# Performance work log

Measured on AMD Instinct MI355X. Metric: run time of the kernel, lower is better.

Reference implementation:

```python
import jax, jax.numpy as jnp
import numpy as np

B, T, D, H = 2, 2048, 1024, 16  # batch, seq_len, d_model (d_in==d_out), num_heads
HD = D // H  # head_dim = 64


def setup_inputs() -> dict:
    key = jax.random.key(0)
    ks = jax.random.split(key, 6)
    s = 1.0 / np.sqrt(D)
    return {
        "x": jax.random.normal(ks[0], (B, T, D), dtype=jnp.float32),
        "wq": jax.random.normal(ks[1], (D, D), dtype=jnp.float32) * s,
        "wk": jax.random.normal(ks[2], (D, D), dtype=jnp.float32) * s,
        "wv": jax.random.normal(ks[3], (D, D), dtype=jnp.float32) * s,
        "wo": jax.random.normal(ks[4], (D, D), dtype=jnp.float32) * s,
        "bo": jax.random.normal(ks[5], (D,), dtype=jnp.float32) * 0.01,
    }


def reference(x, wq, wk, wv, wo, bo):
    b, t, d = x.shape
    # projections (qkv_bias=False), split heads: [b, h, t, hd]
    q = (x @ wq).reshape(b, t, H, HD).transpose(0, 2, 1, 3)
    k = (x @ wk).reshape(b, t, H, HD).transpose(0, 2, 1, 3)
    v = (x @ wv).reshape(b, t, H, HD).transpose(0, 2, 1, 3)
    # causal attention scores [b, h, t, t]
    scores = jnp.einsum("bhqd,bhkd->bhqk", q, k) / jnp.sqrt(jnp.float32(HD))
    causal = jnp.tril(jnp.ones((t, t), dtype=bool))
    scores = jnp.where(causal[None, None, :, :], scores, -jnp.inf)
    attn = jax.nn.softmax(scores, axis=-1)  # dropout p=0.0 -> identity
    ctx = jnp.einsum("bhqk,bhkd->bhqd", attn, v)  # [b, h, t, hd]
    ctx = ctx.transpose(0, 2, 1, 3).reshape(b, t, d)  # merge heads
    return ctx @ wo + bo
```

## Files before the change

### kernel.cpp

```cpp
#include <hip/hip_runtime.h>
#include <hip/hip_bf16.h>
#include <stdint.h>

#define B_  2
#define T_  2048
#define D_  1024
#define H_  16
#define HD_ 64

typedef __bf16 bf16x8 __attribute__((ext_vector_type(8)));
typedef __bf16 bf16x4 __attribute__((ext_vector_type(4)));
typedef float  f32x4  __attribute__((ext_vector_type(4)));

__device__ __forceinline__ void async_copy16(const void* g, void* l) {
  __builtin_amdgcn_global_load_lds((__attribute__((address_space(1))) void*)(g),
                                   (__attribute__((address_space(3))) void*)(l),
                                   16, 0, 0);
}

__global__ void prep_kernel(const float* __restrict__ x,
                            const float* __restrict__ wq, const float* __restrict__ wk,
                            const float* __restrict__ wv, const float* __restrict__ wo,
                            __bf16* __restrict__ xc,
                            __bf16* __restrict__ wqkv_t, __bf16* __restrict__ wo_t) {
  const int id  = blockIdx.x;
  const int tid = threadIdx.x;
  if (id < 4096) {
    __shared__ __bf16 tile[32][33];
    const int z   = id >> 10;
    const int rem = id & 1023;
    const int n0 = (rem & 31) * 32, k0 = (rem >> 5) * 32;
    const int tx = tid & 31, ty = tid >> 5;
    const float* src = (z == 0) ? wq : (z == 1) ? wk : (z == 2) ? wv : wo;
    __bf16* dst = (z < 3) ? (wqkv_t + (size_t)z * 1024 * 1024) : wo_t;
#pragma unroll
    for (int i = 0; i < 4; ++i)
      tile[ty + 8 * i][tx] = (__bf16)src[(size_t)(k0 + ty + 8 * i) * 1024 + n0 + tx];
    __syncthreads();
#pragma unroll
    for (int i = 0; i < 4; ++i)
      dst[(size_t)(n0 + ty + 8 * i) * 1024 + k0 + tx] = tile[tx][ty + 8 * i];
  } else {
    const int i0 = ((id - 4096) * 256 + tid) * 4;
    const f32x4 f = *(const f32x4*)(x + i0);
    bf16x4 v;
#pragma unroll
    for (int k = 0; k < 4; ++k) v[k] = (__bf16)f[k];
    *(bf16x4*)(xc + i0) = v;
  }
}

template <int MODE>
__launch_bounds__(256)
__global__ void gemm128_kernel(const __bf16* __restrict__ A, const __bf16* __restrict__ Bt, int K,
                               __bf16* __restrict__ q_b, __bf16* __restrict__ k_b,
                               __bf16* __restrict__ vt_b,
                               const float* __restrict__ bo, float* __restrict__ outp) {
  __shared__ __align__(16) __bf16 As[128 * 64];
  __shared__ __align__(16) __bf16 Bs[128 * 64];
  const int tid  = threadIdx.x;
  const int w    = tid >> 6, lane = tid & 63;
  const int quad = lane >> 4, lr = lane & 15;

  const int orig = blockIdx.x;
  int bx, by;
  if (MODE == 0) {
    const int wgid = (orig & 7) * 96 + (orig >> 3);
    bx = wgid >> 5;
    by = wgid & 31;
  } else {
    const int wgid = (orig & 7) * 32 + (orig >> 3);
    bx = wgid & 7;
    by = wgid >> 3;
  }
  const int tm = by * 128, tn = bx * 128;
  const int wm = (w >> 1) * 64, wn = (w & 1) * 64;
  const int lrow   = lane >> 3;
  const int gchunk = (lane & 7) ^ lrow;

  f32x4 acc[4][4] = {};

  for (int k0 = 0; k0 < K; k0 += 64) {
#pragma unroll
    for (int c = 0; c < 4; ++c) {
      const int chunk = w * 4 + c;
      const int row   = chunk * 8 + lrow;
      async_copy16(A  + (size_t)(tm + row) * K + k0 + gchunk * 8, As + chunk * 512);
      async_copy16(Bt + (size_t)(tn + row) * K + k0 + gchunk * 8, Bs + chunk * 512);
    }
    __syncthreads();
#pragma unroll
    for (int ks = 0; ks < 2; ++ks) {
      bf16x8 af[4], bfr[4];
#pragma unroll
      for (int mi = 0; mi < 4; ++mi) {
        const int row = wm + mi * 16 + lr;
        const int ch  = (ks * 4 + quad) ^ (row & 7);
        af[mi] = *(const bf16x8*)(As + row * 64 + ch * 8);
      }
#pragma unroll
      for (int ni = 0; ni < 4; ++ni) {
        const int row = wn + ni * 16 + lr;
        const int ch  = (ks * 4 + quad) ^ (row & 7);
        bfr[ni] = *(const bf16x8*)(Bs + row * 64 + ch * 8);
      }
#pragma unroll
      for (int mi = 0; mi < 4; ++mi)
#pragma unroll
        for (int ni = 0; ni < 4; ++ni)
          acc[mi][ni] = __builtin_amdgcn_mfma_f32_16x16x32_bf16(af[mi], bfr[ni], acc[mi][ni], 0, 0, 0);
    }
    __syncthreads();
  }

  if (MODE == 0) {
#pragma unroll
    for (int mi = 0; mi < 4; ++mi) {
      const int mrow0 = tm + wm + mi * 16 + quad * 4;
      const int b  = mrow0 >> 11;
      const int t0 = mrow0 & 2047;
#pragma unroll
      for (int ni = 0; ni < 4; ++ni) {
        const int ncol = tn + wn + ni * 16 + lr;
        const int mat  = ncol >> 10;
        const int nn   = ncol & 1023;
        const int h = nn >> 6, hd = nn & 63;
        if (mat == 0) {
#pragma unroll
          for (int r = 0; r < 4; ++r)
            q_b[((size_t)((b * H_ + h) * T_ + t0 + r)) * HD_ + hd] =
                (__bf16)(acc[mi][ni][r] * 0.125f);
        } else if (mat == 1) {
#pragma unroll
          for (int r = 0; r < 4; ++r)
            k_b[((size_t)((b * H_ + h) * T_ + t0 + r)) * HD_ + hd] =
                (__bf16)(acc[mi][ni][r]);
        } else {
          bf16x4 pk;
#pragma unroll
          for (int r = 0; r < 4; ++r) pk[r] = (__bf16)(acc[mi][ni][r]);
          *(bf16x4*)(vt_b + ((size_t)(b * H_ + h) * HD_ + hd) * T_ + t0) = pk;
        }
      }
    }
  } else {
#pragma unroll
    for (int mi = 0; mi < 4; ++mi) {
      const int m0 = tm + wm + mi * 16 + quad * 4;
#pragma unroll
      for (int ni = 0; ni < 4; ++ni) {
        const int n = tn + wn + ni * 16 + lr;
        const float bias = bo[n];
#pragma unroll
        for (int r = 0; r < 4; ++r)
          outp[(size_t)(m0 + r) * D_ + n] = acc[mi][ni][r] + bias;
      }
    }
  }
}

__launch_bounds__(256, 3)
__global__ void attn_kernel(const __bf16* __restrict__ q_b, const __bf16* __restrict__ k_b,
                            const __bf16* __restrict__ vt_b, __bf16* __restrict__ ctx) {
  __shared__ __align__(16) __bf16 sV[64 * 64];
  __shared__ __align__(16) __bf16 sP[2][64][72];
  const int tid  = threadIdx.x;
  const int w    = tid >> 6, lane = tid & 63;
  const int quad = lane >> 4, lr = lane & 15;
  const int id = blockIdx.x;
  const int bh  = (id & 7) * 4 + ((id >> 3) & 3);
  const int t0i = (id >> 5) & 7;
  const int rnd = id >> 8;
  const int tq  = (3 - rnd) * 8 + ((rnd & 1) ? t0i : (7 - t0i));
  const __bf16* qh = q_b  + (size_t)bh * T_ * HD_;
  const __bf16* kh = k_b  + (size_t)bh * T_ * HD_;
  const __bf16* vh = vt_b + (size_t)bh * HD_ * T_;
  const int b = bh >> 4, h = bh & 15;

  const int r0 = tid >> 3, r1 = (tid + 256) >> 3;
  const int g0 = tid & 7;

  const int q0 = tq * 64;
  const int nj = tq + 1;
  const int w16 = w * 16;

  bf16x8 qf[4][2];
#pragma unroll
  for (int qs = 0; qs < 4; ++qs)
#pragma unroll
    for (int ks = 0; ks < 2; ++ks)
      qf[qs][ks] = *(const bf16x8*)(qh + (size_t)(q0 + qs * 16 + lr) * HD_ + ks * 32 + quad * 8);

  bf16x8 onesf;
#pragma unroll
  for (int j = 0; j < 8; ++j) onesf[j] = (__bf16)1.0f;

  f32x4 o[4] = {};
  f32x4 ls = {};

  const __bf16* kr = kh + (size_t)(w16 + lr) * HD_;
  bf16x8 kf0 = *(const bf16x8*)(kr + quad * 8);
  bf16x8 kf1 = *(const bf16x8*)(kr + 32 + quad * 8);
  bf16x8 kn0, kn1;

  bf16x8 vr0 = *(const bf16x8*)(vh + (size_t)r0 * T_ + g0 * 8);
  bf16x8 vr1 = *(const bf16x8*)(vh + (size_t)r1 * T_ + g0 * 8);

  for (int j = 0; j < nj; ++j) {
    const int j0 = j * 64;
    const int pb = j & 1;
    __syncthreads();
    *(bf16x8*)(sV + r0 * 64 + (g0 ^ (r0 & 7)) * 8) = vr0;
    *(bf16x8*)(sV + r1 * 64 + (g0 ^ (r1 & 7)) * 8) = vr1;
    __syncthreads();
    if (j + 1 < nj) {
      const int jn = j0 + 64;
      vr0 = *(const bf16x8*)(vh + (size_t)r0 * T_ + jn + g0 * 8);
      vr1 = *(const bf16x8*)(vh + (size_t)r1 * T_ + jn + g0 * 8);
      kn0 = *(const bf16x8*)(kr + (size_t)jn * HD_ + quad * 8);
      kn1 = *(const bf16x8*)(kr + (size_t)jn * HD_ + 32 + quad * 8);
    }
    f32x4 ns[4] = {};
    __builtin_amdgcn_s_setprio(1);
#pragma unroll
    for (int qb = 0; qb < 4; ++qb) {
      ns[qb] = __builtin_amdgcn_mfma_f32_16x16x32_bf16(kf0, qf[qb][0], ns[qb], 0, 0, 0);
      ns[qb] = __builtin_amdgcn_mfma_f32_16x16x32_bf16(kf1, qf[qb][1], ns[qb], 0, 0, 0);
    }
    __builtin_amdgcn_s_setprio(0);
    if (j + 1 < nj) { kf0 = kn0; kf1 = kn1; }
    if (j0 + 63 > q0) {
      const int kvb = j0 + w16 + quad * 4;
#pragma unroll
      for (int qb = 0; qb < 4; ++qb) {
        const int qg = q0 + qb * 16 + lr;
#pragma unroll
        for (int r = 0; r < 4; ++r)
          if (kvb + r > qg) ns[qb][r] = -3.0e38f;
      }
    }
#pragma unroll
    for (int qb = 0; qb < 4; ++qb)
#pragma unroll
      for (int r = 0; r < 4; ++r)
        ns[qb][r] = __expf(ns[qb][r]);
#pragma unroll
    for (int qb = 0; qb < 4; ++qb) {
      bf16x4 pk;
#pragma unroll
      for (int r = 0; r < 4; ++r) pk[r] = (__bf16)ns[qb][r];
      *(bf16x4*)(&sP[pb][qb * 16 + lr][w16 + quad * 4]) = pk;
    }
    __syncthreads();
    bf16x8 pf[2];
#pragma unroll
    for (int ks = 0; ks < 2; ++ks)
      pf[ks] = *(const bf16x8*)(&sP[pb][w16 + lr][ks * 32 + quad * 8]);
    __builtin_amdgcn_s_setprio(1);
#pragma unroll
    for (int ni = 0; ni < 4; ++ni) {
      const int row = ni * 16 + lr;
#pragma unroll
      for (int ks = 0; ks < 2; ++ks) {
        const int ch = (ks * 4 + quad) ^ (row & 7);
        bf16x8 vf = *(const bf16x8*)(sV + row * 64 + ch * 8);
        o[ni] = __builtin_amdgcn_mfma_f32_16x16x32_bf16(pf[ks], vf, o[ni], 0, 0, 0);
      }
    }
    ls = __builtin_amdgcn_mfma_f32_16x16x32_bf16(pf[0], onesf, ls, 0, 0, 0);
    ls = __builtin_amdgcn_mfma_f32_16x16x32_bf16(pf[1], onesf, ls, 0, 0, 0);
    __builtin_amdgcn_s_setprio(0);
  }
#pragma unroll
  for (int r = 0; r < 4; ++r) {
    const float inv = 1.0f / ls[r];
    const int t = q0 + w16 + quad * 4 + r;
#pragma unroll
    for (int ni = 0; ni < 4; ++ni)
      ctx[((size_t)(b * T_ + t)) * D_ + h * HD_ + ni * 16 + lr] =
          (__bf16)(o[ni][r] * inv);
  }
}

extern "C" void kernel_launch(void* const* d_in, const int* in_sizes, int n_in,
                              void* d_out, int out_size, void* d_ws, size_t ws_size,
                              hipStream_t stream) {
  (void)in_sizes; (void)n_in; (void)out_size; (void)ws_size;
  const float* x  = (const float*)d_in[0];
  const float* wq = (const float*)d_in[1];
  const float* wk = (const float*)d_in[2];
  const float* wv = (const float*)d_in[3];
  const float* wo = (const float*)d_in[4];
  const float* bo = (const float*)d_in[5];
  float* outp = (float*)d_out;

  char* ws = (char*)d_ws;
  __bf16* ctx    = (__bf16*)(ws + 0);
  __bf16* wqkv_t = (__bf16*)(ws + 0);
  __bf16* wo_t   = (__bf16*)(ws + 8388608);
  __bf16* q_b    = (__bf16*)(ws + 10485760);
  __bf16* k_b    = (__bf16*)(ws + 18874368);
  __bf16* vt_b   = (__bf16*)(ws + 27262976);
  __bf16* xc     = (__bf16*)(ws + 35651584);

  prep_kernel<<<8192, 256, 0, stream>>>(x, wq, wk, wv, wo, xc, wqkv_t, wo_t);
  gemm128_kernel<0><<<768, 256, 0, stream>>>(xc, wqkv_t, 1024, q_b, k_b, vt_b, nullptr, nullptr);
  attn_kernel<<<1024, 256, 0, stream>>>(q_b, k_b, vt_b, ctx);
  gemm128_kernel<1><<<256, 256, 0, stream>>>(ctx, wo_t, 1024, nullptr, nullptr, nullptr, bo, outp);
}
```

Before: 172.3 us.

## Software-pipeline attention loop: compute next QK^T scores during current PV step

Restructures the attention inner loop so the QK^T MFMAs for the next KV tile are issued in the same iteration as the current tile's PV MFMAs. V is now double-buffered in LDS, which cuts the per-iteration barriers from three to one. K fragments are prefetched two tiles ahead in alternating register sets. The aim is to overlap exp/softmax work with MFMA and to remove synchronization stalls, at the cost of extra LDS and register pressure under the 3-blocks-per-SM launch bound.

Result: slower. 183.2 us (+6.3%).

```diff
diff --git a/kernel.cpp b/kernel.cpp
--- a/kernel.cpp
+++ b/kernel.cpp
@@ -162,7 +162,7 @@
 __launch_bounds__(256, 3)
 __global__ void attn_kernel(const __bf16* __restrict__ q_b, const __bf16* __restrict__ k_b,
                             const __bf16* __restrict__ vt_b, __bf16* __restrict__ ctx) {
-  __shared__ __align__(16) __bf16 sV[64 * 64];
+  __shared__ __align__(16) __bf16 sV[2][64 * 64];
   __shared__ __align__(16) __bf16 sP[2][64][72];
   const int tid  = threadIdx.x;
   const int w    = tid >> 6, lane = tid & 63;
@@ -199,63 +199,79 @@
   f32x4 ls = {};
 
   const __bf16* kr = kh + (size_t)(w16 + lr) * HD_;
-  bf16x8 kf0 = *(const bf16x8*)(kr + quad * 8);
-  bf16x8 kf1 = *(const bf16x8*)(kr + 32 + quad * 8);
-  bf16x8 kn0, kn1;
-
+  bf16x8 kA0 = *(const bf16x8*)(kr + quad * 8);
+  bf16x8 kA1 = *(const bf16x8*)(kr + 32 + quad * 8);
+  bf16x8 kB0, kB1;
+  if (nj > 1) {
+    kB0 = *(const bf16x8*)(kr + (size_t)64 * HD_ + quad * 8);
+    kB1 = *(const bf16x8*)(kr + (size_t)64 * HD_ + 32 + quad * 8);
+  }
   bf16x8 vr0 = *(const bf16x8*)(vh + (size_t)r0 * T_ + g0 * 8);
   bf16x8 vr1 = *(const bf16x8*)(vh + (size_t)r1 * T_ + g0 * 8);
+
+  f32x4 ns[4] = {};
+  __builtin_amdgcn_s_setprio(1);
+#pragma unroll
+  for (int qb = 0; qb < 4; ++qb) {
+    ns[qb] = __builtin_amdgcn_mfma_f32_16x16x32_bf16(kA0, qf[qb][0], ns[qb], 0, 0, 0);
+    ns[qb] = __builtin_amdgcn_mfma_f32_16x16x32_bf16(kA1, qf[qb][1], ns[qb], 0, 0, 0);
+  }
+  __builtin_amdgcn_s_setprio(0);
 
   for (int j = 0; j < nj; ++j) {
     const int j0 = j * 64;
     const int pb = j & 1;
-    __syncthreads();
-    *(bf16x8*)(sV + r0 * 64 + (g0 ^ (r0 & 7)) * 8) = vr0;
-    *(bf16x8*)(sV + r1 * 64 + (g0 ^ (r1 & 7)) * 8) = vr1;
+    if (j == nj - 1) {
+      const int kvb = j0 + w16 + quad * 4;
+#pragma unroll
+      for (int qb = 0; qb < 4; ++qb) {
+        const int qg = q0 + qb * 16 + lr;
+#pragma unroll
+        for (int r = 0; r < 4; ++r)
+          if (kvb + r > qg) ns[qb][r] = -3.0e38f;
+      }
+    }
+#pragma unroll
+    for (int qb = 0; qb < 4; ++qb)
+#pragma unroll
+      for (int r = 0; r < 4; ++r)
+        ns[qb][r] = __expf(ns[qb][r]);
+#pragma unroll
+    for (int qb = 0; qb < 4; ++qb) {
+      bf16x4 pk;
+#pragma unroll
+      for (int r = 0; r < 4; ++r) pk[r] = (__bf16)ns[qb][r];
+      *(bf16x4*)(&sP[pb][qb * 16 + lr][w16 + quad * 4]) = pk;
+    }
+    *(bf16x8*)(&sV[pb][r0 * 64 + (g0 ^ (r0 & 7)) * 8]) = vr0;
+    *(bf16x8*)(&sV[pb][r1 * 64 + (g0 ^ (r1 & 7)) * 8]) = vr1;
     __syncthreads();
     if (j + 1 < nj) {
       const int jn = j0 + 64;
       vr0 = *(const bf16x8*)(vh + (size_t)r0 * T_ + jn + g0 * 8);
       vr1 = *(const bf16x8*)(vh + (size_t)r1 * T_ + jn + g0 * 8);
-      kn0 = *(const bf16x8*)(kr + (size_t)jn * HD_ + quad * 8);
-      kn1 = *(const bf16x8*)(kr + (size_t)jn * HD_ + 32 + quad * 8);
-    }
-    f32x4 ns[4] = {};
-    __builtin_amdgcn_s_setprio(1);
-#pragma unroll
-    for (int qb = 0; qb < 4; ++qb) {
-      ns[qb] = __builtin_amdgcn_mfma_f32_16x16x32_bf16(kf0, qf[qb][0], ns[qb], 0, 0, 0);
-      ns[qb] = __builtin_amdgcn_mfma_f32_16x16x32_bf16(kf1, qf[qb][1], ns[qb], 0, 0, 0);
-    }
-    __builtin_amdgcn_s_setprio(0);
-    if (j + 1 < nj) { kf0 = kn0; kf1 = kn1; }
-    if (j0 + 63 > q0) {
-      const int kvb = j0 + w16 + quad * 4;
-#pragma unroll
-      for (int qb = 0; qb < 4; ++qb) {
-        const int qg = q0 + qb * 16 + lr;
-#pragma unroll
-        for (int r = 0; r < 4; ++r)
-          if (kvb + r > qg) ns[qb][r] = -3.0e38f;
-      }
-    }
-#pragma unroll
-    for (int qb = 0; qb < 4; ++qb)
-#pragma unroll
-      for (int r = 0; r < 4; ++r)
-        ns[qb][r] = __expf(ns[qb][r]);
-#pragma unroll
-    for (int qb = 0; qb < 4; ++qb) {
-      bf16x4 pk;
-#pragma unroll
-      for (int r = 0; r < 4; ++r) pk[r] = (__bf16)ns[qb][r];
-      *(bf16x4*)(&sP[pb][qb * 16 + lr][w16 + quad * 4]) = pk;
-    }
-    __syncthreads();
+    }
+    if (j + 2 < nj) {
+      const size_t j2 = (size_t)(j0 + 128) * HD_;
+      if (j & 1) { kB0 = *(const bf16x8*)(kr + j2 + quad * 8);
+                   kB1 = *(const bf16x8*)(kr + j2 + 32 + quad * 8); }
+      else       { kA0 = *(const bf16x8*)(kr + j2 + quad * 8);
+                   kA1 = *(const bf16x8*)(kr + j2 + 32 + quad * 8); }
+    }
     bf16x8 pf[2];
 #pragma unroll
     for (int ks = 0; ks < 2; ++ks)
       pf[ks] = *(const bf16x8*)(&sP[pb][w16 + lr][ks * 32 + quad * 8]);
+    if (j + 1 < nj) {
+      const bf16x8 k0 = (j & 1) ? kA0 : kB0;
+      const bf16x8 k1 = (j & 1) ? kA1 : kB1;
+#pragma unroll
+      for (int qb = 0; qb < 4; ++qb) {
+        f32x4 z = {};
+        z = __builtin_amdgcn_mfma_f32_16x16x32_bf16(k0, qf[qb][0], z, 0, 0, 0);
+        ns[qb] = __builtin_amdgcn_mfma_f32_16x16x32_bf16(k1, qf[qb][1], z, 0, 0, 0);
+      }
+    }
     __builtin_amdgcn_s_setprio(1);
 #pragma unroll
     for (int ni = 0; ni < 4; ++ni) {
@@ -263,7 +279,7 @@
 #pragma unroll
       for (int ks = 0; ks < 2; ++ks) {
         const int ch = (ks * 4 + quad) ^ (row & 7);
-        bf16x8 vf = *(const bf16x8*)(sV + row * 64 + ch * 8);
+        bf16x8 vf = *(const bf16x8*)(&sV[pb][row * 64 + ch * 8]);
         o[ni] = __builtin_amdgcn_mfma_f32_16x16x32_bf16(pf[ks], vf, o[ni], 0, 0, 0);
       }
     }
```

## Split KV across waves in attention, removing per-tile LDS exchange and barriers

Applied to the files above, without the earlier changes.

The attention kernel now has each wave own a 16-key slice of every 64-key tile. The P·V product uses 16x16x16 MFMAs fed directly from the score registers, with V loaded from global into registers, so the sP/sV shared-memory staging and the three barriers per KV tile are gone. K/V loads are double-buffered in registers. Each wave's partial output and row sums are reduced once through LDS at the end. This raises register and LDS use (launch bounds drop to 2 blocks per SM) and adds a final cross-wave reduction.

After: 195.0 us. +13.2%, slower.

```diff
diff --git a/kernel.cpp b/kernel.cpp
--- a/kernel.cpp
+++ b/kernel.cpp
@@ -11,6 +11,7 @@
 typedef __bf16 bf16x8 __attribute__((ext_vector_type(8)));
 typedef __bf16 bf16x4 __attribute__((ext_vector_type(4)));
 typedef float  f32x4  __attribute__((ext_vector_type(4)));
+typedef short  s16x4  __attribute__((ext_vector_type(4)));
 
 __device__ __forceinline__ void async_copy16(const void* g, void* l) {
   __builtin_amdgcn_global_load_lds((__attribute__((address_space(1))) void*)(g),
@@ -159,11 +160,11 @@
   }
 }
 
-__launch_bounds__(256, 3)
+__launch_bounds__(256, 2)
 __global__ void attn_kernel(const __bf16* __restrict__ q_b, const __bf16* __restrict__ k_b,
                             const __bf16* __restrict__ vt_b, __bf16* __restrict__ ctx) {
-  __shared__ __align__(16) __bf16 sV[64 * 64];
-  __shared__ __align__(16) __bf16 sP[2][64][72];
+  __shared__ __align__(16) float sO[4][64][68];
+  __shared__ float sLS[4][64];
   const int tid  = threadIdx.x;
   const int w    = tid >> 6, lane = tid & 63;
   const int quad = lane >> 4, lr = lane & 15;
@@ -177,9 +178,6 @@
   const __bf16* vh = vt_b + (size_t)bh * HD_ * T_;
   const int b = bh >> 4, h = bh & 15;
 
-  const int r0 = tid >> 3, r1 = (tid + 256) >> 3;
-  const int g0 = tid & 7;
-
   const int q0 = tq * 64;
   const int nj = tq + 1;
   const int w16 = w * 16;
@@ -191,46 +189,39 @@
     for (int ks = 0; ks < 2; ++ks)
       qf[qs][ks] = *(const bf16x8*)(qh + (size_t)(q0 + qs * 16 + lr) * HD_ + ks * 32 + quad * 8);
 
-  bf16x8 onesf;
-#pragma unroll
-  for (int j = 0; j < 8; ++j) onesf[j] = (__bf16)1.0f;
-
-  f32x4 o[4] = {};
-  f32x4 ls = {};
-
-  const __bf16* kr = kh + (size_t)(w16 + lr) * HD_;
-  bf16x8 kf0 = *(const bf16x8*)(kr + quad * 8);
-  bf16x8 kf1 = *(const bf16x8*)(kr + 32 + quad * 8);
-  bf16x8 kn0, kn1;
-
-  bf16x8 vr0 = *(const bf16x8*)(vh + (size_t)r0 * T_ + g0 * 8);
-  bf16x8 vr1 = *(const bf16x8*)(vh + (size_t)r1 * T_ + g0 * 8);
-
-  for (int j = 0; j < nj; ++j) {
-    const int j0 = j * 64;
-    const int pb = j & 1;
-    __syncthreads();
-    *(bf16x8*)(sV + r0 * 64 + (g0 ^ (r0 & 7)) * 8) = vr0;
-    *(bf16x8*)(sV + r1 * 64 + (g0 ^ (r1 & 7)) * 8) = vr1;
-    __syncthreads();
-    if (j + 1 < nj) {
-      const int jn = j0 + 64;
-      vr0 = *(const bf16x8*)(vh + (size_t)r0 * T_ + jn + g0 * 8);
-      vr1 = *(const bf16x8*)(vh + (size_t)r1 * T_ + jn + g0 * 8);
-      kn0 = *(const bf16x8*)(kr + (size_t)jn * HD_ + quad * 8);
-      kn1 = *(const bf16x8*)(kr + (size_t)jn * HD_ + 32 + quad * 8);
-    }
+  const s16x4 ones16 = {0x3F80, 0x3F80, 0x3F80, 0x3F80};
+
+  f32x4 ot[4][4] = {};
+  f32x4 lsa[4]   = {};
+
+  const __bf16* kbase = kh + (size_t)(w16 + lr) * HD_ + quad * 8;
+  const __bf16* vbase = vh + (size_t)lr * T_ + w16 + quad * 4;
+
+  auto LK = [&](int j, bf16x8& k0, bf16x8& k1) {
+    const __bf16* p = kbase + (size_t)j * 64 * HD_;
+    k0 = *(const bf16x8*)p;
+    k1 = *(const bf16x8*)(p + 32);
+  };
+  auto LV = [&](int j, s16x4& v0, s16x4& v1, s16x4& v2, s16x4& v3) {
+    const __bf16* p = vbase + j * 64;
+    v0 = *(const s16x4*)(p);
+    v1 = *(const s16x4*)(p + 16 * T_);
+    v2 = *(const s16x4*)(p + 32 * T_);
+    v3 = *(const s16x4*)(p + 48 * T_);
+  };
+
+  auto TILE = [&](int j, const bf16x8& k0, const bf16x8& k1,
+                  const s16x4& v0, const s16x4& v1, const s16x4& v2, const s16x4& v3) {
     f32x4 ns[4] = {};
     __builtin_amdgcn_s_setprio(1);
 #pragma unroll
     for (int qb = 0; qb < 4; ++qb) {
-      ns[qb] = __builtin_amdgcn_mfma_f32_16x16x32_bf16(kf0, qf[qb][0], ns[qb], 0, 0, 0);
-      ns[qb] = __builtin_amdgcn_mfma_f32_16x16x32_bf16(kf1, qf[qb][1], ns[qb], 0, 0, 0);
+      ns[qb] = __builtin_amdgcn_mfma_f32_16x16x32_bf16(k0, qf[qb][0], ns[qb], 0, 0, 0);
+      ns[qb] = __builtin_amdgcn_mfma_f32_16x16x32_bf16(k1, qf[qb][1], ns[qb], 0, 0, 0);
     }
     __builtin_amdgcn_s_setprio(0);
-    if (j + 1 < nj) { kf0 = kn0; kf1 = kn1; }
-    if (j0 + 63 > q0) {
-      const int kvb = j0 + w16 + quad * 4;
+    if (j == nj - 1) {
+      const int kvb = j * 64 + w16 + quad * 4;
 #pragma unroll
       for (int qb = 0; qb < 4; ++qb) {
         const int qg = q0 + qb * 16 + lr;
@@ -239,46 +230,68 @@
           if (kvb + r > qg) ns[qb][r] = -3.0e38f;
       }
     }
+    s16x4 pb[4];
+#pragma unroll
+    for (int qb = 0; qb < 4; ++qb) {
+      bf16x4 t;
+#pragma unroll
+      for (int r = 0; r < 4; ++r) t[r] = (__bf16)__expf(ns[qb][r]);
+      pb[qb] = __builtin_bit_cast(s16x4, t);
+    }
+    const s16x4 vv[4] = {v0, v1, v2, v3};
+    __builtin_amdgcn_s_setprio(1);
+#pragma unroll
+    for (int hb = 0; hb < 4; ++hb)
+#pragma unroll
+      for (int qb = 0; qb < 4; ++qb)
+        ot[hb][qb] = __builtin_amdgcn_mfma_f32_16x16x16bf16_1k(vv[hb], pb[qb], ot[hb][qb], 0, 0, 0);
 #pragma unroll
     for (int qb = 0; qb < 4; ++qb)
-#pragma unroll
-      for (int r = 0; r < 4; ++r)
-        ns[qb][r] = __expf(ns[qb][r]);
-#pragma unroll
-    for (int qb = 0; qb < 4; ++qb) {
-      bf16x4 pk;
-#pragma unroll
-      for (int r = 0; r < 4; ++r) pk[r] = (__bf16)ns[qb][r];
-      *(bf16x4*)(&sP[pb][qb * 16 + lr][w16 + quad * 4]) = pk;
-    }
-    __syncthreads();
-    bf16x8 pf[2];
-#pragma unroll
-    for (int ks = 0; ks < 2; ++ks)
-      pf[ks] = *(const bf16x8*)(&sP[pb][w16 + lr][ks * 32 + quad * 8]);
-    __builtin_amdgcn_s_setprio(1);
-#pragma unroll
-    for (int ni = 0; ni < 4; ++ni) {
-      const int row = ni * 16 + lr;
-#pragma unroll
-      for (int ks = 0; ks < 2; ++ks) {
-        const int ch = (ks * 4 + quad) ^ (row & 7);
-        bf16x8 vf = *(const bf16x8*)(sV + row * 64 + ch * 8);
-        o[ni] = __builtin_amdgcn_mfma_f32_16x16x32_bf16(pf[ks], vf, o[ni], 0, 0, 0);
-      }
-    }
-    ls = __builtin_amdgcn_mfma_f32_16x16x32_bf16(pf[0], onesf, ls, 0, 0, 0);
-    ls = __builtin_amdgcn_mfma_f32_16x16x32_bf16(pf[1], onesf, ls, 0, 0, 0);
+      lsa[qb] = __builtin_amdgcn_mfma_f32_16x16x16bf16_1k(ones16, pb[qb], lsa[qb], 0, 0, 0);
     __builtin_amdgcn_s_setprio(0);
-  }
-#pragma unroll
-  for (int r = 0; r < 4; ++r) {
-    const float inv = 1.0f / ls[r];
-    const int t = q0 + w16 + quad * 4 + r;
-#pragma unroll
-    for (int ni = 0; ni < 4; ++ni)
-      ctx[((size_t)(b * T_ + t)) * D_ + h * HD_ + ni * 16 + lr] =
-          (__bf16)(o[ni][r] * inv);
+  };
+
+  bf16x8 ka0, ka1, kb0, kb1;
+  s16x4  va0, va1, va2, va3, vb0, vb1, vb2, vb3;
+  LK(0, ka0, ka1);
+  LV(0, va0, va1, va2, va3);
+  for (int j = 0; j < nj; ) {
+    if (j + 1 < nj) { LK(j + 1, kb0, kb1); LV(j + 1, vb0, vb1, vb2, vb3); }
+    TILE(j, ka0, ka1, va0, va1, va2, va3);
+    ++j; if (j >= nj) break;
+    if (j + 1 < nj) { LK(j + 1, ka0, ka1); LV(j + 1, va0, va1, va2, va3); }
+    TILE(j, kb0, kb1, vb0, vb1, vb2, vb3);
+    ++j;
+  }
+
+#pragma unroll
+  for (int hb = 0; hb < 4; ++hb)
+#pragma unroll
+    for (int qb = 0; qb < 4; ++qb)
+      *(f32x4*)&sO[w][qb * 16 + lr][hb * 16 + quad * 4] = ot[hb][qb];
+  if (quad == 0) {
+#pragma unroll
+    for (int qb = 0; qb < 4; ++qb)
+      sLS[w][qb * 16 + lr] = lsa[qb][0];
+  }
+  __syncthreads();
+  const float lsq = sLS[0][w16 + lr] + sLS[1][w16 + lr]
+                  + sLS[2][w16 + lr] + sLS[3][w16 + lr];
+  const float inv = 1.0f / lsq;
+  const int t = q0 + w16 + lr;
+#pragma unroll
+  for (int hb = 0; hb < 4; ++hb) {
+    f32x4 of = *(const f32x4*)&sO[0][w16 + lr][hb * 16 + quad * 4];
+#pragma unroll
+    for (int ww = 1; ww < 4; ++ww) {
+      const f32x4 pv = *(const f32x4*)&sO[ww][w16 + lr][hb * 16 + quad * 4];
+#pragma unroll
+      for (int r = 0; r < 4; ++r) of[r] += pv[r];
+    }
+    bf16x4 pk;
+#pragma unroll
+    for (int r = 0; r < 4; ++r) pk[r] = (__bf16)(of[r] * inv);
+    *(bf16x4*)(ctx + ((size_t)(b * T_ + t)) * D_ + h * HD_ + hb * 16 + quad * 4) = pk;
   }
 }
 
```
